# Optimization experiments

Hardware: AMD Instinct MI355X
Metric: run time of the kernel (lower is better)

The kernel has to match this reference:

```python
import jax, jax.numpy as jnp
import numpy as np

EMBED = 768
N_HEADS = 12
HEAD = EMBED // N_HEADS  # 64
B, T = 2, 2048


def setup_inputs() -> dict:
    key = jax.random.key(0)
    ks = jax.random.split(key, 5)
    s = 0.02
    return {
        "x": jax.random.normal(ks[0], (B, T, EMBED), dtype=jnp.float32),
        "w_attn": jax.random.normal(ks[1], (EMBED, 3 * EMBED), dtype=jnp.float32) * s,
        "b_attn": jnp.zeros((3 * EMBED,), dtype=jnp.float32),
        "w_proj": jax.random.normal(ks[2], (EMBED, EMBED), dtype=jnp.float32) * s,
        "b_proj": jnp.zeros((EMBED,), dtype=jnp.float32),
    }


def reference(x, w_attn, b_attn, w_proj, b_proj):
    b, t, c = x.shape
    scale = HEAD ** -0.5
    qkv = x @ w_attn + b_attn  # [b,t,3c]
    q, k, v = jnp.split(qkv, 3, axis=-1)

    # einops 'b t (h n) -> b n t h' with n=N_HEADS: channel dim factors as
    # (head_size, n_heads) — head index is the inner factor.
    def split_heads(u):
        return u.reshape(b, t, HEAD, N_HEADS).transpose(0, 3, 1, 2)  # [b,n,t,h]

    q, k, v = split_heads(q), split_heads(k), split_heads(v)

    scores = jnp.einsum("bnth,bnsh->bnts", q, k) * scale  # [b,n,t,t]
    causal = jnp.tril(jnp.ones((t, t), dtype=bool))
    scores = jnp.where(causal, scores, jnp.finfo(scores.dtype).min)
    weights = jax.nn.softmax(scores, axis=-1)
    att = jnp.einsum("bnts,bnsh->bnth", weights, v)  # [b,n,t,h]

    # 'b n t h -> b t (n h)': heads are the OUTER factor on output
    att = att.transpose(0, 2, 1, 3).reshape(b, t, c)
    return att @ w_proj + b_proj
```

## Files before the change

kernel.cpp:

```cpp
#include <hip/hip_runtime.h>
#include <hip/hip_bf16.h>
#include <math.h>

#define NB      2
#define T_SZ    2048
#define EMBEDC  768
#define NHEADS  12
#define HEADD   64
#define QKV_PER (NB * NHEADS * T_SZ * HEADD)
#define QSCALE  0.18033688011112042f

typedef __bf16 bf16x8 __attribute__((ext_vector_type(8)));
typedef float  f32x4  __attribute__((ext_vector_type(4)));
typedef float  f32x16 __attribute__((ext_vector_type(16)));

__device__ inline ushort f2bf(float x) {
    union { float f; uint u; } v; v.f = x;
    uint r = v.u + 0x7fffu + ((v.u >> 16) & 1u);
    return (ushort)(r >> 16);
}

__device__ inline uint pack2bf(float a, float b) {
    union { __bf16 h[2]; uint u; } t;
    t.h[0] = (__bf16)a; t.h[1] = (__bf16)b;
    return t.u;
}

__device__ inline void gload16(const ushort* g, ushort* l) {
    __builtin_amdgcn_global_load_lds(
        (const __attribute__((address_space(1))) unsigned int*)g,
        (__attribute__((address_space(3))) unsigned int*)l, 16, 0, 0);
}

__global__ __launch_bounds__(256) void cast_k(const float* __restrict__ in,
                                              ushort* __restrict__ out, int n)
{
    int i = (blockIdx.x * 256 + threadIdx.x) * 8;
    if (i >= n) return;
    float4 a = *(const float4*)(in + i);
    float4 b = *(const float4*)(in + i + 4);
    union { ushort u[8]; int4 v; } p;
    p.u[0] = f2bf(a.x); p.u[1] = f2bf(a.y); p.u[2] = f2bf(a.z); p.u[3] = f2bf(a.w);
    p.u[4] = f2bf(b.x); p.u[5] = f2bf(b.y); p.u[6] = f2bf(b.z); p.u[7] = f2bf(b.w);
    *(int4*)(out + i) = p.v;
}

template <int PERM>
__global__ __launch_bounds__(256) void tcast_k(const float* __restrict__ in,
                                               ushort* __restrict__ out,
                                               int R, int C)
{
    __shared__ float t[32][33];
    const int c0 = blockIdx.x * 32, r0 = blockIdx.y * 32;
    const int tx = threadIdx.x & 31, ty = threadIdx.x >> 5;
#pragma unroll
    for (int u = 0; u < 4; ++u)
        t[ty + 8 * u][tx] = in[(size_t)(r0 + ty + 8 * u) * C + c0 + tx];
    __syncthreads();
#pragma unroll
    for (int u = 0; u < 4; ++u) {
        int n = c0 + ty + 8 * u;
        int orow = n;
        if (PERM) {
            int mat = n / EMBEDC, cc = n % EMBEDC;
            orow = mat * EMBEDC + (cc % NHEADS) * HEADD + cc / NHEADS;
        }
        out[(size_t)orow * R + r0 + tx] = f2bf(t[tx][ty + 8 * u]);
    }
}

__global__ __launch_bounds__(256) void vt_k(const ushort* __restrict__ in,
                                            ushort* __restrict__ out)
{
    __shared__ ushort tile[64][66];
    const int bh = blockIdx.y;
    const int t0 = blockIdx.x * 64;
    const int tid = threadIdx.x;
#pragma unroll
    for (int u = 0; u < 2; ++u) {
        int s = tid + 256 * u;
        int r = s >> 3, c8 = s & 7;
        *(bf16x8*)&tile[r][c8 * 8] =
            *(const bf16x8*)(in + ((size_t)bh * T_SZ + t0 + r) * HEADD + c8 * 8);
    }
    __syncthreads();
#pragma unroll
    for (int u = 0; u < 2; ++u) {
        int s = tid + 256 * u;
        int hd = s >> 3, tt = s & 7;
        union { ushort v[8]; int4 q; } pk;
#pragma unroll
        for (int j = 0; j < 8; ++j) pk.v[j] = tile[tt * 8 + j][hd];
        *(int4*)(out + ((size_t)bh * HEADD + hd) * T_SZ + t0 + tt * 8) = pk.q;
    }
}

#define STAGE(buf, koff)                                        \
    do {                                                        \
        gload16(gA0 + (koff), &As[buf][lA0o]);                  \
        gload16(gA1 + (koff), &As[buf][lA1o]);                  \
        gload16(gB0 + (koff), &Bs[buf][lB0o]);                  \
        gload16(gB1 + (koff), &Bs[buf][lB1o]);                  \
    } while (0)

template <int MODE>
__global__ __launch_bounds__(256) void gemm_bf16_k(
    const ushort* __restrict__ A, const ushort* __restrict__ Bt,
    const float* __restrict__ bias, void* __restrict__ outp,
    int M, int N, int K)
{
    __shared__ ushort As[2][128 * 32];
    __shared__ ushort Bs[2][128 * 32];

    const int tid = threadIdx.x;
    const int w = tid >> 6, l = tid & 63;
    const int g = l >> 4, r16 = l & 15;
    const int wr = w >> 1, wc = w & 1;
    const int m0 = blockIdx.y * 128, n0 = blockIdx.x * 128;

    const int srow = l >> 2;
    const int scol = ((l & 3) ^ (srow & 3)) * 8;
    const ushort* gA0 = A + (size_t)(m0 + 32 * w + srow) * K + scol;
    const ushort* gA1 = gA0 + (size_t)16 * K;
    const ushort* gB0 = Bt + (size_t)(n0 + 32 * w + srow) * K + scol;
    const ushort* gB1 = gB0 + (size_t)16 * K;
    const int lA0o = (32 * w) * 32,      lA1o = (32 * w + 16) * 32;
    const int lB0o = lA0o,               lB1o = lA1o;

    f32x4 acc[4][4];
#pragma unroll
    for (int i = 0; i < 4; ++i)
#pragma unroll
        for (int j = 0; j < 4; ++j) acc[i][j] = (f32x4){0.f, 0.f, 0.f, 0.f};

    const int rck = (r16 & 3);

    STAGE(0, 0);
    __syncthreads();

    int cur = 0;
    for (int k0 = 0; k0 < K; k0 += 32) {
        if (k0 + 32 < K) STAGE(cur ^ 1, k0 + 32);

        const ushort* sA = As[cur];
        const ushort* sB = Bs[cur];
        bf16x8 af[4], bfr[4];
#pragma unroll
        for (int ms = 0; ms < 4; ++ms) {
            int row = 64 * wr + 16 * ms + r16;
            af[ms] = *(const bf16x8*)&sA[row * 32 + ((g ^ rck) * 8)];
        }
#pragma unroll
        for (int ns = 0; ns < 4; ++ns) {
            int row = 64 * wc + 16 * ns + r16;
            bfr[ns] = *(const bf16x8*)&sB[row * 32 + ((g ^ rck) * 8)];
        }
#pragma unroll
        for (int ms = 0; ms < 4; ++ms)
#pragma unroll
            for (int ns = 0; ns < 4; ++ns)
                acc[ms][ns] = __builtin_amdgcn_mfma_f32_16x16x32_bf16(
                    af[ms], bfr[ns], acc[ms][ns], 0, 0, 0);

        __syncthreads();
        cur ^= 1;
    }

#pragma unroll
    for (int ns = 0; ns < 4; ++ns) {
        const int n = n0 + 64 * wc + 16 * ns + r16;
        if (MODE == 0) {
            float* out = (float*)outp;
            const float bv = bias[n];
#pragma unroll
            for (int ms = 0; ms < 4; ++ms) {
                const int mb = m0 + 64 * wr + 16 * ms + 4 * g;
#pragma unroll
                for (int r = 0; r < 4; ++r)
                    out[(size_t)(mb + r) * N + n] = acc[ms][ns][r] + bv;
            }
        } else {
            ushort* ob = (ushort*)outp;
            const int mat  = n / EMBEDC;
            const int c    = n - mat * EMBEDC;
            const int head = c >> 6;
            const int hd   = c & 63;
            const float bv = bias[mat * EMBEDC + hd * NHEADS + head];
            const float qs = (mat == 0) ? QSCALE : 1.f;
#pragma unroll
            for (int ms = 0; ms < 4; ++ms) {
                const int mb = m0 + 64 * wr + 16 * ms + 4 * g;
#pragma unroll
                for (int r = 0; r < 4; ++r) {
                    const int m = mb + r;
                    const int b = m >> 11, t = m & 2047;
                    const size_t bh = (size_t)(b * NHEADS + head);
                    ob[(size_t)mat * QKV_PER + (bh * T_SZ + t) * HEADD + hd] =
                        f2bf((acc[ms][ns][r] + bv) * qs);
                }
            }
        }
    }
}

__global__ __launch_bounds__(64) void attn_mfma_k(
    const ushort* __restrict__ Qb, const ushort* __restrict__ Kb,
    const ushort* __restrict__ Vtb, ushort* __restrict__ Out)
{
    const int bid = blockIdx.x;
    const int xcd = bid & 7, jj = bid >> 3;
    const int bh = xcd * 3 + (jj >> 5);
    const int p  = jj & 31;
    const int bb = bh / NHEADS, head = bh % NHEADS;
    const int l = threadIdx.x;
    const int q31 = l & 31, hi = l >> 5;
    const ushort* Qg = Qb + (size_t)bh * T_SZ * HEADD;
    const ushort* Kg = Kb + (size_t)bh * T_SZ * HEADD;
    const ushort* Vg = Vtb + (size_t)bh * HEADD * T_SZ;

    const ushort* V0 = Vg + (size_t)q31 * T_SZ + 8 * hi;
    const ushort* V1 = Vg + (size_t)(32 + q31) * T_SZ + 8 * hi;

    for (int rep = 0; rep < 2; ++rep) {
        const int iq = rep ? (63 - p) : p;
        const int q0 = iq * 32;
        const int nt = iq + 1;

        const ushort* qrow = Qg + (size_t)(q0 + q31) * HEADD + 8 * hi;
        const bf16x8 qf0 = *(const bf16x8*)(qrow);
        const bf16x8 qf1 = *(const bf16x8*)(qrow + 16);
        const bf16x8 qf2 = *(const bf16x8*)(qrow + 32);
        const bf16x8 qf3 = *(const bf16x8*)(qrow + 48);

        f32x16 o0, o1, z;
#pragma unroll
        for (int r = 0; r < 16; ++r) { o0[r] = 0.f; o1[r] = 0.f; z[r] = 0.f; }
        float mR = -1e30f, lR = 0.f;

        const ushort* Krow = Kg + (size_t)q31 * HEADD + 8 * hi;
        bf16x8 kf0 = *(const bf16x8*)(Krow);
        bf16x8 kf1 = *(const bf16x8*)(Krow + 16);
        bf16x8 kf2 = *(const bf16x8*)(Krow + 32);
        bf16x8 kf3 = *(const bf16x8*)(Krow + 48);

        for (int kt = 0; kt < nt; ++kt) {
            const int kvb = kt * 32;
            const bf16x8 va0 = *(const bf16x8*)(V0 + kvb);
            const bf16x8 va1 = *(const bf16x8*)(V0 + kvb + 16);
            const bf16x8 vb0 = *(const bf16x8*)(V1 + kvb);
            const bf16x8 vb1 = *(const bf16x8*)(V1 + kvb + 16);
            bf16x8 kn0, kn1, kn2, kn3;
            if (kt + 1 < nt) {
                const ushort* kr = Krow + (size_t)(kvb + 32) * HEADD;
                kn0 = *(const bf16x8*)(kr);
                kn1 = *(const bf16x8*)(kr + 16);
                kn2 = *(const bf16x8*)(kr + 32);
                kn3 = *(const bf16x8*)(kr + 48);
            }

            f32x16 st = z;
            st = __builtin_amdgcn_mfma_f32_32x32x16_bf16(kf0, qf0, st, 0, 0, 0);
            st = __builtin_amdgcn_mfma_f32_32x32x16_bf16(kf1, qf1, st, 0, 0, 0);
            st = __builtin_amdgcn_mfma_f32_32x32x16_bf16(kf2, qf2, st, 0, 0, 0);
            st = __builtin_amdgcn_mfma_f32_32x32x16_bf16(kf3, qf3, st, 0, 0, 0);

            if (kt == nt - 1) {
#pragma unroll
                for (int r = 0; r < 16; ++r)
                    if (((r & 3) + 8 * (r >> 2) + 4 * hi) > q31)
                        st[r] = -1e30f;
            }

            float pm = st[0];
#pragma unroll
            for (int r = 1; r < 16; ++r) pm = fmaxf(pm, st[r]);
            pm = fmaxf(pm, __shfl_xor(pm, 32));
            if (!__all(pm - mR <= 8.f)) {
                float mNew = fmaxf(mR, pm);
                float sc = exp2f(mR - mNew);
                lR *= sc;
                o0 *= sc;
                o1 *= sc;
                mR = mNew;
            }
            float rs = 0.f;
#pragma unroll
            for (int r = 0; r < 16; ++r) {
                float e = exp2f(st[r] - mR);
                st[r] = e;
                rs += e;
            }
            rs += __shfl_xor(rs, 32);
            lR += rs;

            uint w0 = pack2bf(st[0],  st[1]),  w1 = pack2bf(st[2],  st[3]);
            uint w2 = pack2bf(st[4],  st[5]),  w3 = pack2bf(st[6],  st[7]);
            uint w4 = pack2bf(st[8],  st[9]),  w5 = pack2bf(st[10], st[11]);
            uint w6 = pack2bf(st[12], st[13]), w7 = pack2bf(st[14], st[15]);

            uint e0 = (uint)__shfl_xor((int)(hi ? w0 : w2), 32);
            uint e1 = (uint)__shfl_xor((int)(hi ? w1 : w3), 32);
            uint e2 = (uint)__shfl_xor((int)(hi ? w4 : w6), 32);
            uint e3 = (uint)__shfl_xor((int)(hi ? w5 : w7), 32);

            union { uint u[4]; bf16x8 v; } b0, b1;
            b0.u[0] = hi ? e0 : w0;  b0.u[1] = hi ? e1 : w1;
            b0.u[2] = hi ? w2 : e0;  b0.u[3] = hi ? w3 : e1;
            b1.u[0] = hi ? e2 : w4;  b1.u[1] = hi ? e3 : w5;
            b1.u[2] = hi ? w6 : e2;  b1.u[3] = hi ? w7 : e3;

            o0 = __builtin_amdgcn_mfma_f32_32x32x16_bf16(va0, b0.v, o0, 0, 0, 0);
            o0 = __builtin_amdgcn_mfma_f32_32x32x16_bf16(va1, b1.v, o0, 0, 0, 0);
            o1 = __builtin_amdgcn_mfma_f32_32x32x16_bf16(vb0, b0.v, o1, 0, 0, 0);
            o1 = __builtin_amdgcn_mfma_f32_32x32x16_bf16(vb1, b1.v, o1, 0, 0, 0);

            kf0 = kn0; kf1 = kn1; kf2 = kn2; kf3 = kn3;
        }

        const float inv = 1.f / lR;
        ushort* orow = Out + ((size_t)(bb * T_SZ + q0 + q31)) * EMBEDC
                     + head * HEADD + 4 * hi;
#pragma unroll
        for (int c = 0; c < 4; ++c) {
            uint2 pv0, pv1;
            pv0.x = pack2bf(o0[4 * c + 0] * inv, o0[4 * c + 1] * inv);
            pv0.y = pack2bf(o0[4 * c + 2] * inv, o0[4 * c + 3] * inv);
            pv1.x = pack2bf(o1[4 * c + 0] * inv, o1[4 * c + 1] * inv);
            pv1.y = pack2bf(o1[4 * c + 2] * inv, o1[4 * c + 3] * inv);
            *(uint2*)(orow + 8 * c)      = pv0;
            *(uint2*)(orow + 32 + 8 * c) = pv1;
        }
    }
}

extern "C" void kernel_launch(void* const* d_in, const int* in_sizes, int n_in,
                              void* d_out, int out_size, void* d_ws, size_t ws_size,
                              hipStream_t stream)
{
    const float* x      = (const float*)d_in[0];
    const float* w_attn = (const float*)d_in[1];
    const float* b_attn = (const float*)d_in[2];
    const float* w_proj = (const float*)d_in[3];
    const float* b_proj = (const float*)d_in[4];
    float* out = (float*)d_out;

    ushort* qw   = (ushort*)d_ws;
    ushort* vT   = qw + (size_t)3 * QKV_PER;
    ushort* attb = vT + QKV_PER;
    ushort* xb   = attb + QKV_PER;
    ushort* waT  = xb + QKV_PER;
    ushort* wpT  = waT + (size_t)EMBEDC * 3 * EMBEDC;

    cast_k<<<QKV_PER / (256 * 8), 256, 0, stream>>>(x, xb, QKV_PER);
    tcast_k<1><<<dim3(3 * EMBEDC / 32, EMBEDC / 32), 256, 0, stream>>>(
        w_attn, waT, EMBEDC, 3 * EMBEDC);
    tcast_k<0><<<dim3(EMBEDC / 32, EMBEDC / 32), 256, 0, stream>>>(
        w_proj, wpT, EMBEDC, EMBEDC);

    gemm_bf16_k<1><<<dim3(2304 / 128, 4096 / 128), 256, 0, stream>>>(
        xb, waT, b_attn, qw, NB * T_SZ, 3 * EMBEDC, EMBEDC);

    vt_k<<<dim3(T_SZ / 64, NB * NHEADS), 256, 0, stream>>>(
        qw + 2 * (size_t)QKV_PER, vT);

    attn_mfma_k<<<768, 64, 0, stream>>>(
        qw, qw + QKV_PER, vT, attb);

    gemm_bf16_k<0><<<dim3(768 / 128, 4096 / 128), 256, 0, stream>>>(
        attb, wpT, b_proj, out, NB * T_SZ, EMBEDC, EMBEDC);
}
```

Measured before the change: 132.2 us.

## Split attention KV loop across four waves with LDS softmax merge

The attention kernel now launches one 256-thread block per 32-row query tile instead of one wave handling two paired tiles. The four waves each take a contiguous chunk of KV tiles, then combine their partial outputs, running maxima and sums through shared memory with a swizzled layout before writing bf16 output. This raises parallelism and evens out the causal-triangle imbalance. The cost is 32KB+ of LDS per block, a barrier and merge step, and idle waves on short rows.

```diff
diff --git a/kernel.cpp b/kernel.cpp
--- a/kernel.cpp
+++ b/kernel.cpp
@@ -203,54 +203,60 @@
     }
 }
 
-__global__ __launch_bounds__(64) void attn_mfma_k(
+__global__ __launch_bounds__(256) void attn_mfma_k(
     const ushort* __restrict__ Qb, const ushort* __restrict__ Kb,
     const ushort* __restrict__ Vtb, ushort* __restrict__ Out)
 {
+    __shared__ float fsm[4 * 2048];
+    __shared__ float Ml[128], Ll[128];
+
     const int bid = blockIdx.x;
-    const int xcd = bid & 7, jj = bid >> 3;
-    const int bh = xcd * 3 + (jj >> 5);
-    const int p  = jj & 31;
+    const int xcd = bid & 7, j = bid >> 3;
+    const int bh = xcd * 3 + (j >> 6);
+    const int iq = 63 - (j & 63);
     const int bb = bh / NHEADS, head = bh % NHEADS;
-    const int l = threadIdx.x;
+    const int tid = threadIdx.x;
+    const int w = tid >> 6, l = tid & 63;
     const int q31 = l & 31, hi = l >> 5;
+    const int q0 = iq * 32;
+    const int nt = iq + 1;
+    const int cpw = (nt + 3) >> 2;
+    const int b0 = w * cpw;
+    const int b1 = min(b0 + cpw, nt);
+
     const ushort* Qg = Qb + (size_t)bh * T_SZ * HEADD;
     const ushort* Kg = Kb + (size_t)bh * T_SZ * HEADD;
     const ushort* Vg = Vtb + (size_t)bh * HEADD * T_SZ;
-
     const ushort* V0 = Vg + (size_t)q31 * T_SZ + 8 * hi;
     const ushort* V1 = Vg + (size_t)(32 + q31) * T_SZ + 8 * hi;
 
-    for (int rep = 0; rep < 2; ++rep) {
-        const int iq = rep ? (63 - p) : p;
-        const int q0 = iq * 32;
-        const int nt = iq + 1;
-
+    f32x16 o0, o1, z;
+#pragma unroll
+    for (int r = 0; r < 16; ++r) { o0[r] = 0.f; o1[r] = 0.f; z[r] = 0.f; }
+    float mR = -1e30f, lR = 0.f;
+
+    if (b0 < b1) {
         const ushort* qrow = Qg + (size_t)(q0 + q31) * HEADD + 8 * hi;
         const bf16x8 qf0 = *(const bf16x8*)(qrow);
         const bf16x8 qf1 = *(const bf16x8*)(qrow + 16);
         const bf16x8 qf2 = *(const bf16x8*)(qrow + 32);
         const bf16x8 qf3 = *(const bf16x8*)(qrow + 48);
 
-        f32x16 o0, o1, z;
-#pragma unroll
-        for (int r = 0; r < 16; ++r) { o0[r] = 0.f; o1[r] = 0.f; z[r] = 0.f; }
-        float mR = -1e30f, lR = 0.f;
-
         const ushort* Krow = Kg + (size_t)q31 * HEADD + 8 * hi;
-        bf16x8 kf0 = *(const bf16x8*)(Krow);
-        bf16x8 kf1 = *(const bf16x8*)(Krow + 16);
-        bf16x8 kf2 = *(const bf16x8*)(Krow + 32);
-        bf16x8 kf3 = *(const bf16x8*)(Krow + 48);
-
-        for (int kt = 0; kt < nt; ++kt) {
+        const ushort* kr0 = Krow + (size_t)(b0 * 32) * HEADD;
+        bf16x8 kf0 = *(const bf16x8*)(kr0);
+        bf16x8 kf1 = *(const bf16x8*)(kr0 + 16);
+        bf16x8 kf2 = *(const bf16x8*)(kr0 + 32);
+        bf16x8 kf3 = *(const bf16x8*)(kr0 + 48);
+
+        for (int kt = b0; kt < b1; ++kt) {
             const int kvb = kt * 32;
             const bf16x8 va0 = *(const bf16x8*)(V0 + kvb);
             const bf16x8 va1 = *(const bf16x8*)(V0 + kvb + 16);
             const bf16x8 vb0 = *(const bf16x8*)(V1 + kvb);
             const bf16x8 vb1 = *(const bf16x8*)(V1 + kvb + 16);
             bf16x8 kn0, kn1, kn2, kn3;
-            if (kt + 1 < nt) {
+            if (kt + 1 < b1) {
                 const ushort* kr = Krow + (size_t)(kvb + 32) * HEADD;
                 kn0 = *(const bf16x8*)(kr);
                 kn1 = *(const bf16x8*)(kr + 16);
@@ -303,33 +309,63 @@
             uint e2 = (uint)__shfl_xor((int)(hi ? w4 : w6), 32);
             uint e3 = (uint)__shfl_xor((int)(hi ? w5 : w7), 32);
 
-            union { uint u[4]; bf16x8 v; } b0, b1;
-            b0.u[0] = hi ? e0 : w0;  b0.u[1] = hi ? e1 : w1;
-            b0.u[2] = hi ? w2 : e0;  b0.u[3] = hi ? w3 : e1;
-            b1.u[0] = hi ? e2 : w4;  b1.u[1] = hi ? e3 : w5;
-            b1.u[2] = hi ? w6 : e2;  b1.u[3] = hi ? w7 : e3;
-
-            o0 = __builtin_amdgcn_mfma_f32_32x32x16_bf16(va0, b0.v, o0, 0, 0, 0);
-            o0 = __builtin_amdgcn_mfma_f32_32x32x16_bf16(va1, b1.v, o0, 0, 0, 0);
-            o1 = __builtin_amdgcn_mfma_f32_32x32x16_bf16(vb0, b0.v, o1, 0, 0, 0);
-            o1 = __builtin_amdgcn_mfma_f32_32x32x16_bf16(vb1, b1.v, o1, 0, 0, 0);
+            union { uint u[4]; bf16x8 v; } p0, p1;
+            p0.u[0] = hi ? e0 : w0;  p0.u[1] = hi ? e1 : w1;
+            p0.u[2] = hi ? w2 : e0;  p0.u[3] = hi ? w3 : e1;
+            p1.u[0] = hi ? e2 : w4;  p1.u[1] = hi ? e3 : w5;
+            p1.u[2] = hi ? w6 : e2;  p1.u[3] = hi ? w7 : e3;
+
+            o0 = __builtin_amdgcn_mfma_f32_32x32x16_bf16(va0, p0.v, o0, 0, 0, 0);
+            o0 = __builtin_amdgcn_mfma_f32_32x32x16_bf16(va1, p1.v, o0, 0, 0, 0);
+            o1 = __builtin_amdgcn_mfma_f32_32x32x16_bf16(vb0, p0.v, o1, 0, 0, 0);
+            o1 = __builtin_amdgcn_mfma_f32_32x32x16_bf16(vb1, p1.v, o1, 0, 0, 0);
 
             kf0 = kn0; kf1 = kn1; kf2 = kn2; kf3 = kn3;
         }
-
-        const float inv = 1.f / lR;
-        ushort* orow = Out + ((size_t)(bb * T_SZ + q0 + q31)) * EMBEDC
-                     + head * HEADD + 4 * hi;
-#pragma unroll
-        for (int c = 0; c < 4; ++c) {
-            uint2 pv0, pv1;
-            pv0.x = pack2bf(o0[4 * c + 0] * inv, o0[4 * c + 1] * inv);
-            pv0.y = pack2bf(o0[4 * c + 2] * inv, o0[4 * c + 3] * inv);
-            pv1.x = pack2bf(o1[4 * c + 0] * inv, o1[4 * c + 1] * inv);
-            pv1.y = pack2bf(o1[4 * c + 2] * inv, o1[4 * c + 3] * inv);
-            *(uint2*)(orow + 8 * c)      = pv0;
-            *(uint2*)(orow + 32 + 8 * c) = pv1;
-        }
+    }
+
+    if (hi == 0) {
+        Ml[w * 32 + q31] = mR;
+        Ll[w * 32 + q31] = lR;
+    }
+    const int key = 4 * (q31 & 15);
+    float* img = &fsm[w * 2048 + q31 * 64];
+#pragma unroll
+    for (int c = 0; c < 4; ++c) {
+        f32x4 s0 = {o0[4 * c + 0], o0[4 * c + 1], o0[4 * c + 2], o0[4 * c + 3]};
+        f32x4 s1 = {o1[4 * c + 0], o1[4 * c + 1], o1[4 * c + 2], o1[4 * c + 3]};
+        *(f32x4*)&img[(8 * c + 4 * hi) ^ key]        = s0;
+        *(f32x4*)&img[((8 * c + 4 * hi) + 32) ^ key] = s1;
+    }
+    __syncthreads();
+
+    {
+        const int q  = tid >> 3;
+        const int dc = tid & 7;
+        const int gkey = 4 * (q & 15);
+        float m0 = Ml[q], m1 = Ml[32 + q], m2 = Ml[64 + q], m3 = Ml[96 + q];
+        float mt = fmaxf(fmaxf(m0, m1), fmaxf(m2, m3));
+        float f0 = exp2f(m0 - mt), f1 = exp2f(m1 - mt);
+        float f2 = exp2f(m2 - mt), f3 = exp2f(m3 - mt);
+        float lt = Ll[q] * f0 + Ll[32 + q] * f1 + Ll[64 + q] * f2 + Ll[96 + q] * f3;
+        const float inv = 1.f / lt;
+        const float* row = &fsm[q * 64];
+        f32x4 acc[2];
+#pragma unroll
+        for (int jj = 0; jj < 2; ++jj) {
+            const int dsw = (dc * 8 + 4 * jj) ^ gkey;
+            acc[jj] = *(const f32x4*)&row[dsw] * f0
+                    + *(const f32x4*)&row[2048 + dsw] * f1
+                    + *(const f32x4*)&row[4096 + dsw] * f2
+                    + *(const f32x4*)&row[6144 + dsw] * f3;
+        }
+        uint4 pv;
+        pv.x = pack2bf(acc[0][0] * inv, acc[0][1] * inv);
+        pv.y = pack2bf(acc[0][2] * inv, acc[0][3] * inv);
+        pv.z = pack2bf(acc[1][0] * inv, acc[1][1] * inv);
+        pv.w = pack2bf(acc[1][2] * inv, acc[1][3] * inv);
+        *(uint4*)(Out + ((size_t)(bb * T_SZ + q0 + q)) * EMBEDC
+                  + head * HEADD + dc * 8) = pv;
     }
 }
 
@@ -363,7 +399,7 @@
     vt_k<<<dim3(T_SZ / 64, NB * NHEADS), 256, 0, stream>>>(
         qw + 2 * (size_t)QKV_PER, vT);
 
-    attn_mfma_k<<<768, 64, 0, stream>>>(
+    attn_mfma_k<<<1536, 256, 0, stream>>>(
         qw, qw + QKV_PER, vT, attb);
 
     gemm_bf16_k<0><<<dim3(768 / 128, 4096 / 128), 256, 0, stream>>>(
```

Result: faster. 124.3 us (-6.0%).
